# Kernel optimization log

Measured on AMD Instinct MI355X. Metric: run time of the kernel, lower is better.

Reference implementation:

```python
import jax, jax.numpy as jnp
import numpy as np

NUM_NODES = 100000
NUM_EDGES = 1600000
NUM_GRAPHS = 64
IN_CH, HID, NCLS = 15, 128, 11


def setup_inputs() -> dict:
    key = jax.random.key(0)
    ks = jax.random.split(key, 9)
    x = jax.random.normal(ks[0], (NUM_NODES, IN_CH), dtype=jnp.float32)
    edge_index = jax.random.randint(ks[1], (2, NUM_EDGES), 0, NUM_NODES, dtype=jnp.int64)
    batch = jnp.sort(jax.random.randint(ks[2], (NUM_NODES,), 0, NUM_GRAPHS, dtype=jnp.int64))
    s1 = 1.0 / np.sqrt(IN_CH)
    s2 = 1.0 / np.sqrt(HID)
    W1 = jax.random.normal(ks[3], (IN_CH, HID), dtype=jnp.float32) * s1
    b1 = jax.random.normal(ks[4], (HID,), dtype=jnp.float32) * s1
    W2 = jax.random.normal(ks[5], (HID, HID), dtype=jnp.float32) * s2
    b2 = jax.random.normal(ks[6], (HID,), dtype=jnp.float32) * s2
    Wf = jax.random.normal(ks[7], (HID, NCLS), dtype=jnp.float32) * s2
    bf = jax.random.normal(ks[8], (NCLS,), dtype=jnp.float32) * s2
    return {"x": x, "edge_index": edge_index, "batch": batch,
            "W1": W1, "b1": b1, "W2": W2, "b2": b2, "Wf": Wf, "bf": bf}


def reference(x, edge_index, batch, W1, b1, W2, b2, Wf, bf):
    N = x.shape[0]
    loop = jnp.arange(N, dtype=edge_index.dtype)
    # PyG GCNConv: add self-loops, symmetric D^{-1/2} A D^{-1/2} normalization
    src = jnp.concatenate([edge_index[0], loop])
    dst = jnp.concatenate([edge_index[1], loop])
    deg = jax.ops.segment_sum(jnp.ones(src.shape[0], dtype=x.dtype), dst, num_segments=N)
    dinv = deg ** -0.5  # deg >= 1 due to self-loops
    norm = (dinv[src] * dinv[dst])[:, None]  # [E+N, 1]

    def gcn(h, W, b):
        m = h @ W                                   # transform first (smaller gather)
        agg = jax.ops.segment_sum(m[src] * norm, dst, num_segments=N)
        return agg + b

    h = jax.nn.relu(gcn(x, W1, b1))
    h = jax.nn.relu(gcn(h, W2, b2))

    # global_mean_pool over graph ids
    sums = jax.ops.segment_sum(h, batch, num_segments=NUM_GRAPHS)
    cnts = jax.ops.segment_sum(jnp.ones((N,), dtype=h.dtype), batch, num_segments=NUM_GRAPHS)
    pooled = sums / jnp.maximum(cnts, 1.0)[:, None]  # [G, HID]
    return pooled @ Wf + bf                          # [G, NCLS]
```

## Files before the change

### kernel.cpp

```cpp
#include <hip/hip_runtime.h>

#define N_NODES 100000
#define N_EDGES 1600000
#define N_GRAPHS 64
#define IN_CH 15
#define HID 128
#define NCLS 11

#define NBUCK 196
#define NBF 512
#define EPB (N_EDGES / NBF)

using short8 = __attribute__((ext_vector_type(8))) short;
using f32x4 = __attribute__((ext_vector_type(4))) float;
using f32x2 = __attribute__((ext_vector_type(2))) float;

__device__ __forceinline__ unsigned short f2bf(float f) {
    unsigned u = __builtin_bit_cast(unsigned, f);
    u += 0x7FFF + ((u >> 16) & 1);
    return (unsigned short)(u >> 16);
}
__device__ __forceinline__ unsigned packbf(float a, float b) {
    return (unsigned)f2bf(a) | ((unsigned)f2bf(b) << 16);
}
__device__ __forceinline__ float2 unpackbf(unsigned v) {
    float2 r;
    unsigned lo = v << 16;
    unsigned hi = v & 0xFFFF0000u;
    r.x = __builtin_bit_cast(float, lo);
    r.y = __builtin_bit_cast(float, hi);
    return r;
}

__device__ __forceinline__ unsigned char f2fp8(float f) {
    return (unsigned char)(__builtin_amdgcn_cvt_pk_fp8_f32(f, f, 0, false) & 0xFF);
}

__global__ __launch_bounds__(256) void k_init(float* __restrict__ pooled) {
    int i = blockIdx.x * 256 + threadIdx.x;
    if (i < N_GRAPHS * HID) pooled[i] = 0.f;
}

__global__ __launch_bounds__(256) void k_hist(const int* __restrict__ dst,
                                              int* __restrict__ cntm) {
    __shared__ int hist[NBUCK];
    int t = threadIdx.x;
    for (int i = t; i < NBUCK; i += 256) hist[i] = 0;
    __syncthreads();
    int base = blockIdx.x * EPB;
#pragma unroll
    for (int i = 0; i < (EPB + 255) / 256; ++i) {
        int e = i * 256 + t;
        if (e < EPB) atomicAdd(&hist[dst[base + e] >> 9], 1);
    }
    __syncthreads();
    for (int b = t; b < NBUCK; b += 256)
        cntm[b * NBF + blockIdx.x] = hist[b];
}

__global__ __launch_bounds__(256) void k_btot(const int* __restrict__ cntm,
                                              int* __restrict__ tot) {
    __shared__ int red[256];
    int b = blockIdx.x, t = threadIdx.x;
    red[t] = cntm[b * NBF + t] + cntm[b * NBF + t + 256];
    __syncthreads();
    for (int off = 128; off > 0; off >>= 1) {
        if (t < off) red[t] += red[t + off];
        __syncthreads();
    }
    if (t == 0) tot[b] = red[0];
}

__global__ __launch_bounds__(256) void k_bscan(const int* __restrict__ tot,
                                               int* __restrict__ bbase,
                                               int* __restrict__ rowptr) {
    __shared__ int arr[256];
    int t = threadIdx.x;
    arr[t] = (t < NBUCK) ? tot[t] : 0;
    __syncthreads();
    for (int off = 1; off < 256; off <<= 1) {
        int v = (t >= off) ? arr[t - off] : 0;
        __syncthreads();
        arr[t] += v;
        __syncthreads();
    }
    if (t < NBUCK) bbase[t] = (t == 0) ? 0 : arr[t - 1];
    if (t == 0) rowptr[N_NODES] = N_EDGES;
}

__global__ __launch_bounds__(NBF) void k_offs(const int* __restrict__ cntm,
                                              const int* __restrict__ bbase,
                                              int* __restrict__ offs) {
    __shared__ int arr[NBF];
    int b = blockIdx.x, t = threadIdx.x;
    arr[t] = cntm[b * NBF + t];
    __syncthreads();
    for (int off = 1; off < NBF; off <<= 1) {
        int v = (t >= off) ? arr[t - off] : 0;
        __syncthreads();
        arr[t] += v;
        __syncthreads();
    }
    offs[b * NBF + t] = bbase[b] + ((t == 0) ? 0 : arr[t - 1]);
}

__global__ __launch_bounds__(256) void k_partition(const int* __restrict__ src,
                                                   const int* __restrict__ dst,
                                                   const int* __restrict__ offs,
                                                   unsigned* __restrict__ staging) {
    __shared__ int cur[NBUCK];
    int t = threadIdx.x;
    for (int b = t; b < NBUCK; b += 256) cur[b] = offs[b * NBF + blockIdx.x];
    __syncthreads();
    int base = blockIdx.x * EPB;
#pragma unroll
    for (int i = 0; i < (EPB + 255) / 256; ++i) {
        int e = i * 256 + t;
        if (e < EPB) {
            int d = dst[base + e];
            int s = src[base + e];
            int slot = atomicAdd(&cur[d >> 9], 1);
            staging[slot] = ((unsigned)(d & 511) << 17) | (unsigned)s;
        }
    }
}

__global__ __launch_bounds__(256) void k_fuse(const unsigned* __restrict__ staging,
                                              const int* __restrict__ bbase,
                                              int* __restrict__ rowptr,
                                              float* __restrict__ dinv,
                                              int* __restrict__ csr_src) {
    __shared__ int cnt[512];
    __shared__ int cur[512];
    __shared__ int arr[256];
    int b = blockIdx.x, t = threadIdx.x;
    cnt[t] = 0; cnt[t + 256] = 0;
    __syncthreads();
    int beg = bbase[b];
    int end = (b == NBUCK - 1) ? N_EDGES : bbase[b + 1];
    for (int e = beg + t; e < end; e += 256)
        atomicAdd(&cnt[staging[e] >> 17], 1);
    __syncthreads();
    int c0 = cnt[2 * t], c1 = cnt[2 * t + 1];
    arr[t] = c0 + c1;
    __syncthreads();
    for (int off = 1; off < 256; off <<= 1) {
        int v = (t >= off) ? arr[t - off] : 0;
        __syncthreads();
        arr[t] += v;
        __syncthreads();
    }
    int excl = (t == 0) ? 0 : arr[t - 1];
    int p0 = beg + excl;
    int p1 = p0 + c0;
    cur[2 * t] = p0;
    cur[2 * t + 1] = p1;
    int n0 = b << 9;
    int n = n0 + 2 * t;
    if (n < N_NODES) { rowptr[n] = p0; dinv[n] = rsqrtf((float)(c0 + 1)); }
    n = n0 + 2 * t + 1;
    if (n < N_NODES) { rowptr[n] = p1; dinv[n] = rsqrtf((float)(c1 + 1)); }
    __syncthreads();
    for (int e = beg + t; e < end; e += 256) {
        unsigned v = staging[e];
        int pos = atomicAdd(&cur[v >> 17], 1);
        csr_src[pos] = (int)(v & 0x1FFFFu);
    }
}

__global__ __launch_bounds__(256) void k_w2pack(const float* __restrict__ W2,
                                                uint4* __restrict__ Bp) {
    int i = blockIdx.x * 256 + threadIdx.x;
    if (i >= 2048) return;
    int lane = i & 63;
    int kb = (i >> 6) & 3;
    int ct = i >> 8;
    int col = ct * 16 + (lane & 15);
    int k0 = kb * 32 + ((lane >> 4) & 3) * 8;
    unsigned w[4];
#pragma unroll
    for (int p = 0; p < 4; ++p) {
        int k = k0 + 2 * p;
        w[p] = packbf(W2[k * HID + col], W2[(k + 1) * HID + col]);
    }
    Bp[i] = make_uint4(w[0], w[1], w[2], w[3]);
}

__global__ __launch_bounds__(256) void k_prescale(const float* __restrict__ x,
                                                  const float* __restrict__ dinv,
                                                  unsigned* __restrict__ xs) {
    int i = blockIdx.x * 256 + threadIdx.x;
    if (i >= N_NODES * 8) return;
    int n = i >> 3, p = i & 7;
    float dv = dinv[n];
    int c0 = 2 * p, c1 = c0 + 1;
    float a = x[(size_t)n * IN_CH + c0] * dv;
    float b = (c1 < IN_CH) ? x[(size_t)n * IN_CH + c1] * dv : 0.f;
    xs[i] = packbf(a, b);
}

__global__ __launch_bounds__(256) void k_gather15(const int* __restrict__ rowptr,
                                                  const int* __restrict__ csr_src,
                                                  const unsigned* __restrict__ xs,
                                                  const float* __restrict__ dinv,
                                                  float* __restrict__ agg) {
    int wave = (blockIdx.x * 256 + threadIdx.x) >> 6;
    if (wave >= N_NODES) return;
    int n = wave;
    int l = threadIdx.x & 63;
    unsigned g = (unsigned)(l >> 3), cp = (unsigned)(l & 7);
    int beg = rowptr[n], end = rowptr[n + 1];
    float2 acc = make_float2(0.f, 0.f);
    for (int e = beg + (int)g; e < end; e += 8) {
        unsigned s = (unsigned)csr_src[e];
        float2 v = unpackbf(xs[s * 8u + cp]);
        acc.x += v.x; acc.y += v.y;
    }
#pragma unroll
    for (int off = 8; off < 64; off <<= 1) {
        acc.x += __shfl_xor(acc.x, off, 64);
        acc.y += __shfl_xor(acc.y, off, 64);
    }
    if (l < 8) {
        float2 s = unpackbf(xs[(unsigned)n * 8u + (unsigned)l]);
        float dv = dinv[n];
        float2 r = make_float2((acc.x + s.x) * dv, (acc.y + s.y) * dv);
        *(float2*)&agg[(unsigned)n * 16u + 2u * (unsigned)l] = r;
    }
}

__global__ __launch_bounds__(256) void k_xform1b(const float* __restrict__ agg,
                                                 const float* __restrict__ W1,
                                                 const float* __restrict__ b1,
                                                 unsigned* __restrict__ h1b) {
    __shared__ float w[IN_CH * HID];
    int t = threadIdx.x;
    for (int i = t; i < IN_CH * HID; i += 256) w[i] = W1[i];
    __syncthreads();
    int node = blockIdx.x * 4 + (t >> 6);
    int lane = t & 63;
    int c = lane * 2;
    const float* ar = agg + (size_t)node * 16;
    float a0 = b1[c], a1 = b1[c + 1];
#pragma unroll
    for (int k = 0; k < IN_CH; ++k) {
        float av = ar[k];
        a0 += av * w[k * HID + c];
        a1 += av * w[k * HID + c + 1];
    }
    h1b[(size_t)node * 64 + lane] = packbf(fmaxf(a0, 0.f), fmaxf(a1, 0.f));
}

__global__ __launch_bounds__(256) void k_xform2(const unsigned* __restrict__ h1b,
                                                const uint4* __restrict__ Bp,
                                                const float* __restrict__ dinv,
                                                unsigned char* __restrict__ mout) {
    int lane = threadIdx.x & 63;
    int wid = threadIdx.x >> 6;
    int row0 = blockIdx.x * 64 + wid * 16;
    int arow = row0 + (lane & 15);
    const uint4* hbase = (const uint4*)h1b;
    uint4 a_u[4];
#pragma unroll
    for (int kb = 0; kb < 4; ++kb)
        a_u[kb] = hbase[(size_t)arow * 16 + kb * 4 + (lane >> 4)];
    int rbase = row0 + (lane >> 4) * 4;
    float dv[4];
#pragma unroll
    for (int j = 0; j < 4; ++j) dv[j] = dinv[min(rbase + j, N_NODES - 1)];
#pragma unroll
    for (int ct = 0; ct < 8; ++ct) {
        f32x4 acc = {0.f, 0.f, 0.f, 0.f};
#pragma unroll
        for (int kb = 0; kb < 4; ++kb) {
            uint4 b_u = Bp[(ct * 4 + kb) * 64 + lane];
            acc = __builtin_amdgcn_mfma_f32_16x16x32_bf16(
                __builtin_bit_cast(short8, a_u[kb]),
                __builtin_bit_cast(short8, b_u), acc, 0, 0, 0);
        }
        int col = ct * 16 + (lane & 15);
#pragma unroll
        for (int j = 0; j < 4; ++j) {
            int r = rbase + j;
            if (r < N_NODES) mout[(size_t)r * HID + col] = f2fp8(acc[j] * dv[j]);
        }
    }
}

__global__ __launch_bounds__(256) void k_gather(const int* __restrict__ rowptr,
                                                const int* __restrict__ csr_src,
                                                const unsigned* __restrict__ m,
                                                const float* __restrict__ bias,
                                                const float* __restrict__ dinv,
                                                unsigned* __restrict__ outh) {
    int wave = (blockIdx.x * 256 + threadIdx.x) >> 6;
    if (wave >= N_NODES) return;
    unsigned n = (unsigned)wave;
    int lane = threadIdx.x & 63;
    int half = lane >> 5;
    unsigned li = (unsigned)(lane & 31);
    int beg = rowptr[n], end = rowptr[n + 1];
    f32x4 acc = {0.f, 0.f, 0.f, 0.f};
    if (half == 0) {
        unsigned u = m[n * 32u + li];
        f32x2 lo = __builtin_amdgcn_cvt_pk_f32_fp8((int)u, false);
        f32x2 hi = __builtin_amdgcn_cvt_pk_f32_fp8((int)u, true);
        acc[0] += lo[0]; acc[1] += lo[1]; acc[2] += hi[0]; acc[3] += hi[1];
    }
    int e = beg + half;
    for (; e + 6 < end; e += 8) {
        unsigned o0 = (unsigned)csr_src[e + 0] * 32u + li;
        unsigned o1 = (unsigned)csr_src[e + 2] * 32u + li;
        unsigned o2 = (unsigned)csr_src[e + 4] * 32u + li;
        unsigned o3 = (unsigned)csr_src[e + 6] * 32u + li;
        unsigned u0 = m[o0];
        unsigned u1 = m[o1];
        unsigned u2 = m[o2];
        unsigned u3 = m[o3];
        f32x2 l0 = __builtin_amdgcn_cvt_pk_f32_fp8((int)u0, false);
        f32x2 h0 = __builtin_amdgcn_cvt_pk_f32_fp8((int)u0, true);
        f32x2 l1 = __builtin_amdgcn_cvt_pk_f32_fp8((int)u1, false);
        f32x2 h1 = __builtin_amdgcn_cvt_pk_f32_fp8((int)u1, true);
        f32x2 l2 = __builtin_amdgcn_cvt_pk_f32_fp8((int)u2, false);
        f32x2 h2 = __builtin_amdgcn_cvt_pk_f32_fp8((int)u2, true);
        f32x2 l3 = __builtin_amdgcn_cvt_pk_f32_fp8((int)u3, false);
        f32x2 h3 = __builtin_amdgcn_cvt_pk_f32_fp8((int)u3, true);
        acc[0] += l0[0] + l1[0] + l2[0] + l3[0];
        acc[1] += l0[1] + l1[1] + l2[1] + l3[1];
        acc[2] += h0[0] + h1[0] + h2[0] + h3[0];
        acc[3] += h0[1] + h1[1] + h2[1] + h3[1];
    }
    for (; e < end; e += 2) {
        unsigned u = m[(unsigned)csr_src[e] * 32u + li];
        f32x2 lo = __builtin_amdgcn_cvt_pk_f32_fp8((int)u, false);
        f32x2 hi = __builtin_amdgcn_cvt_pk_f32_fp8((int)u, true);
        acc[0] += lo[0]; acc[1] += lo[1]; acc[2] += hi[0]; acc[3] += hi[1];
    }
#pragma unroll
    for (int j = 0; j < 4; ++j) acc[j] += __shfl_xor(acc[j], 32, 64);
    if (half == 0) {
        float dv = dinv[n];
        float4 b = *(const float4*)&bias[li * 4u];
        float r0 = fmaxf(acc[0] * dv + b.x, 0.f);
        float r1 = fmaxf(acc[1] * dv + b.y, 0.f);
        float r2 = fmaxf(acc[2] * dv + b.z, 0.f);
        float r3 = fmaxf(acc[3] * dv + b.w, 0.f);
        uint2 ov;
        ov.x = packbf(r0, r1);
        ov.y = packbf(r2, r3);
        *(uint2*)&outh[n * 64u + li * 2u] = ov;
    }
}

__global__ __launch_bounds__(64) void k_cnt(const int* __restrict__ batch,
                                            int* __restrict__ cnt) {
    int g = threadIdx.x;
    if (g >= N_GRAPHS) return;
    int lo0 = 0, hi0 = N_NODES;
    while (lo0 < hi0) { int mid = (lo0 + hi0) >> 1; if (batch[mid] < g) lo0 = mid + 1; else hi0 = mid; }
    int lo1 = lo0, hi1 = N_NODES;
    while (lo1 < hi1) { int mid = (lo1 + hi1) >> 1; if (batch[mid] < g + 1) lo1 = mid + 1; else hi1 = mid; }
    cnt[g] = lo1 - lo0;
}

#define POOL_CHUNK 128
__global__ __launch_bounds__(256) void k_pool(const unsigned* __restrict__ h,
                                              const int* __restrict__ batch,
                                              float* __restrict__ pooled) {
    int t = threadIdx.x;
    int lane = t & 63;
    int grp = t >> 6;
    int start = blockIdx.x * POOL_CHUNK;
    int end = min(start + POOL_CHUNK, N_NODES);
    float2 acc = make_float2(0.f, 0.f);
    int cur = -1;
    for (int n = start + grp; n < end; n += 4) {
        int g = batch[n];
        if (g != cur) {
            if (cur >= 0) {
                atomicAdd(&pooled[cur * HID + lane * 2], acc.x);
                atomicAdd(&pooled[cur * HID + lane * 2 + 1], acc.y);
            }
            acc = make_float2(0.f, 0.f);
            cur = g;
        }
        float2 v = unpackbf(h[(unsigned)n * 64u + (unsigned)lane]);
        acc.x += v.x; acc.y += v.y;
    }
    if (cur >= 0) {
        atomicAdd(&pooled[cur * HID + lane * 2], acc.x);
        atomicAdd(&pooled[cur * HID + lane * 2 + 1], acc.y);
    }
}

__global__ __launch_bounds__(128) void k_final(const float* __restrict__ pooled,
                                               const int* __restrict__ cnt,
                                               const float* __restrict__ Wf,
                                               const float* __restrict__ bf,
                                               float* __restrict__ out) {
    __shared__ float p[HID];
    int g = blockIdx.x, t = threadIdx.x;
    float inv = 1.f / fmaxf((float)cnt[g], 1.f);
    p[t] = pooled[g * HID + t] * inv;
    __syncthreads();
    if (t < NCLS) {
        float acc = bf[t];
        for (int k = 0; k < HID; ++k) acc += p[k] * Wf[k * NCLS + t];
        out[g * NCLS + t] = acc;
    }
}

extern "C" void kernel_launch(void* const* d_in, const int* in_sizes, int n_in,
                              void* d_out, int out_size, void* d_ws, size_t ws_size,
                              hipStream_t stream) {
    const float* x   = (const float*)d_in[0];
    const int*   ei  = (const int*)d_in[1];
    const int*   src = ei;
    const int*   dst = ei + N_EDGES;
    const int*   batch = (const int*)d_in[2];
    const float* W1 = (const float*)d_in[3];
    const float* b1 = (const float*)d_in[4];
    const float* W2 = (const float*)d_in[5];
    const float* b2 = (const float*)d_in[6];
    const float* Wf = (const float*)d_in[7];
    const float* bf = (const float*)d_in[8];
    float* out = (float*)d_out;

    char* ws = (char*)d_ws;
    size_t off = 0;
    unsigned* mbuf = (unsigned*)(ws + off);  off += (size_t)N_NODES * 64 * 4;
    unsigned* h1b = (unsigned*)(ws + off);   off += (size_t)N_NODES * 64 * 4;
    unsigned* h2b = (unsigned*)(ws + off);   off += (size_t)N_NODES * 64 * 4;
    int* csr_src = (int*)(ws + off);         off += (size_t)N_EDGES * 4;
    uint4* Bp = (uint4*)(ws + off);          off += (size_t)2048 * 16;
    float* dinv = (float*)(ws + off);        off += (size_t)N_NODES * 4;
    int* rowptr = (int*)(ws + off);          off += (size_t)(N_NODES + 1) * 4;
    int* cntm = (int*)(ws + off);            off += (size_t)NBUCK * NBF * 4;
    int* offs = (int*)(ws + off);            off += (size_t)NBUCK * NBF * 4;
    int* tot = (int*)(ws + off);             off += (size_t)NBUCK * 4;
    int* bbase = (int*)(ws + off);           off += (size_t)NBUCK * 4;
    float* pooled = (float*)(ws + off);      off += (size_t)N_GRAPHS * HID * 4;
    int* cnt = (int*)(ws + off);             off += (size_t)N_GRAPHS * 4;
    unsigned* staging = h2b;
    unsigned* xs = mbuf;
    float* agg = (float*)(mbuf + (size_t)N_NODES * 8);
    unsigned char* mfp8 = (unsigned char*)mbuf;

    k_init<<<(N_GRAPHS * HID + 255) / 256, 256, 0, stream>>>(pooled);
    k_hist<<<NBF, 256, 0, stream>>>(dst, cntm);
    k_btot<<<NBUCK, 256, 0, stream>>>(cntm, tot);
    k_bscan<<<1, 256, 0, stream>>>(tot, bbase, rowptr);
    k_offs<<<NBUCK, NBF, 0, stream>>>(cntm, bbase, offs);
    k_partition<<<NBF, 256, 0, stream>>>(src, dst, offs, staging);
    k_fuse<<<NBUCK, 256, 0, stream>>>(staging, bbase, rowptr, dinv, csr_src);
    k_w2pack<<<8, 256, 0, stream>>>(W2, Bp);

    k_prescale<<<(N_NODES * 8 + 255) / 256, 256, 0, stream>>>(x, dinv, xs);
    k_gather15<<<(N_NODES + 3) / 4, 256, 0, stream>>>(rowptr, csr_src, xs, dinv, agg);
    k_xform1b<<<N_NODES / 4, 256, 0, stream>>>(agg, W1, b1, h1b);

    k_xform2<<<(N_NODES + 63) / 64, 256, 0, stream>>>(h1b, Bp, dinv, mfp8);
    k_gather<<<(N_NODES + 3) / 4, 256, 0, stream>>>(rowptr, csr_src, (const unsigned*)mfp8, b2, dinv, h2b);

    k_cnt<<<1, 64, 0, stream>>>(batch, cnt);
    k_pool<<<(N_NODES + POOL_CHUNK - 1) / POOL_CHUNK, 256, 0, stream>>>(h2b, batch, pooled);
    k_final<<<N_GRAPHS, 128, 0, stream>>>(pooled, cnt, Wf, bf, out);
}
```

Baseline: 235.1 us.

## Fuse layer-1 gather with W1 transform and fold small kernels into neighbors

Merges the 15-channel neighbor gather and the 15x128 W1 transform into one kernel: after the wave reduction, lanes broadcast the aggregated features with shuffles and each lane computes two output channels from W1 held in registers. This drops the intermediate agg buffer round trip and one launch. The pooled zero-init moves into the scan kernel, and the per-graph count binary search moves into the final kernel, removing two more tiny launches. Each wave now loads W1 into registers itself, which raises register use and repeats weight loads per node.

```diff
diff --git a/kernel.cpp b/kernel.cpp
--- a/kernel.cpp
+++ b/kernel.cpp
@@ -36,11 +36,6 @@
     return (unsigned char)(__builtin_amdgcn_cvt_pk_fp8_f32(f, f, 0, false) & 0xFF);
 }
 
-__global__ __launch_bounds__(256) void k_init(float* __restrict__ pooled) {
-    int i = blockIdx.x * 256 + threadIdx.x;
-    if (i < N_GRAPHS * HID) pooled[i] = 0.f;
-}
-
 __global__ __launch_bounds__(256) void k_hist(const int* __restrict__ dst,
                                               int* __restrict__ cntm) {
     __shared__ int hist[NBUCK];
@@ -73,7 +68,8 @@
 
 __global__ __launch_bounds__(256) void k_bscan(const int* __restrict__ tot,
                                                int* __restrict__ bbase,
-                                               int* __restrict__ rowptr) {
+                                               int* __restrict__ rowptr,
+                                               float* __restrict__ pooled) {
     __shared__ int arr[256];
     int t = threadIdx.x;
     arr[t] = (t < NBUCK) ? tot[t] : 0;
@@ -86,6 +82,7 @@
     }
     if (t < NBUCK) bbase[t] = (t == 0) ? 0 : arr[t - 1];
     if (t == 0) rowptr[N_NODES] = N_EDGES;
+    for (int i = t; i < N_GRAPHS * HID; i += 256) pooled[i] = 0.f;
 }
 
 __global__ __launch_bounds__(NBF) void k_offs(const int* __restrict__ cntm,
@@ -199,19 +196,26 @@
     xs[i] = packbf(a, b);
 }
 
-__global__ __launch_bounds__(256) void k_gather15(const int* __restrict__ rowptr,
-                                                  const int* __restrict__ csr_src,
-                                                  const unsigned* __restrict__ xs,
-                                                  const float* __restrict__ dinv,
-                                                  float* __restrict__ agg) {
+__global__ __launch_bounds__(256) void k_l1fused(const int* __restrict__ rowptr,
+                                                 const int* __restrict__ csr_src,
+                                                 const unsigned* __restrict__ xs,
+                                                 const float* __restrict__ dinv,
+                                                 const float* __restrict__ W1,
+                                                 const float* __restrict__ b1,
+                                                 unsigned* __restrict__ h1b) {
     int wave = (blockIdx.x * 256 + threadIdx.x) >> 6;
     if (wave >= N_NODES) return;
-    int n = wave;
+    unsigned n = (unsigned)wave;
     int l = threadIdx.x & 63;
-    unsigned g = (unsigned)(l >> 3), cp = (unsigned)(l & 7);
+    int g = l >> 3;
+    unsigned cp = (unsigned)(l & 7);
+    float2 w[IN_CH];
+#pragma unroll
+    for (int k = 0; k < IN_CH; ++k) w[k] = *(const float2*)&W1[k * HID + l * 2];
+    float2 bb = *(const float2*)&b1[l * 2];
     int beg = rowptr[n], end = rowptr[n + 1];
     float2 acc = make_float2(0.f, 0.f);
-    for (int e = beg + (int)g; e < end; e += 8) {
+    for (int e = beg + g; e < end; e += 8) {
         unsigned s = (unsigned)csr_src[e];
         float2 v = unpackbf(xs[s * 8u + cp]);
         acc.x += v.x; acc.y += v.y;
@@ -221,34 +225,21 @@
         acc.x += __shfl_xor(acc.x, off, 64);
         acc.y += __shfl_xor(acc.y, off, 64);
     }
-    if (l < 8) {
-        float2 s = unpackbf(xs[(unsigned)n * 8u + (unsigned)l]);
-        float dv = dinv[n];
-        float2 r = make_float2((acc.x + s.x) * dv, (acc.y + s.y) * dv);
-        *(float2*)&agg[(unsigned)n * 16u + 2u * (unsigned)l] = r;
-    }
-}
-
-__global__ __launch_bounds__(256) void k_xform1b(const float* __restrict__ agg,
-                                                 const float* __restrict__ W1,
-                                                 const float* __restrict__ b1,
-                                                 unsigned* __restrict__ h1b) {
-    __shared__ float w[IN_CH * HID];
-    int t = threadIdx.x;
-    for (int i = t; i < IN_CH * HID; i += 256) w[i] = W1[i];
-    __syncthreads();
-    int node = blockIdx.x * 4 + (t >> 6);
-    int lane = t & 63;
-    int c = lane * 2;
-    const float* ar = agg + (size_t)node * 16;
-    float a0 = b1[c], a1 = b1[c + 1];
-#pragma unroll
-    for (int k = 0; k < IN_CH; ++k) {
-        float av = ar[k];
-        a0 += av * w[k * HID + c];
-        a1 += av * w[k * HID + c + 1];
-    }
-    h1b[(size_t)node * 64 + lane] = packbf(fmaxf(a0, 0.f), fmaxf(a1, 0.f));
+    float2 s = unpackbf(xs[n * 8u + cp]);
+    float dv = dinv[n];
+    float ax = (acc.x + s.x) * dv;
+    float ay = (acc.y + s.y) * dv;
+    float a0 = bb.x, a1 = bb.y;
+    int gbase = l & 56;
+#pragma unroll
+    for (int p = 0; p < 8; ++p) {
+        float vx = __shfl(ax, gbase | p, 64);
+        float vy = __shfl(ay, gbase | p, 64);
+        int k0 = 2 * p;
+        a0 += vx * w[k0].x; a1 += vx * w[k0].y;
+        if (k0 + 1 < IN_CH) { a0 += vy * w[k0 + 1].x; a1 += vy * w[k0 + 1].y; }
+    }
+    h1b[(size_t)n * 64 + l] = packbf(fmaxf(a0, 0.f), fmaxf(a1, 0.f));
 }
 
 __global__ __launch_bounds__(256) void k_xform2(const unsigned* __restrict__ h1b,
@@ -350,17 +341,6 @@
         ov.y = packbf(r2, r3);
         *(uint2*)&outh[n * 64u + li * 2u] = ov;
     }
-}
-
-__global__ __launch_bounds__(64) void k_cnt(const int* __restrict__ batch,
-                                            int* __restrict__ cnt) {
-    int g = threadIdx.x;
-    if (g >= N_GRAPHS) return;
-    int lo0 = 0, hi0 = N_NODES;
-    while (lo0 < hi0) { int mid = (lo0 + hi0) >> 1; if (batch[mid] < g) lo0 = mid + 1; else hi0 = mid; }
-    int lo1 = lo0, hi1 = N_NODES;
-    while (lo1 < hi1) { int mid = (lo1 + hi1) >> 1; if (batch[mid] < g + 1) lo1 = mid + 1; else hi1 = mid; }
-    cnt[g] = lo1 - lo0;
 }
 
 #define POOL_CHUNK 128
@@ -394,13 +374,21 @@
 }
 
 __global__ __launch_bounds__(128) void k_final(const float* __restrict__ pooled,
-                                               const int* __restrict__ cnt,
+                                               const int* __restrict__ batch,
                                                const float* __restrict__ Wf,
                                                const float* __restrict__ bf,
                                                float* __restrict__ out) {
     __shared__ float p[HID];
+    __shared__ int bnd[2];
     int g = blockIdx.x, t = threadIdx.x;
-    float inv = 1.f / fmaxf((float)cnt[g], 1.f);
+    if (t < 2) {
+        int key = g + t;
+        int lo = 0, hi = N_NODES;
+        while (lo < hi) { int mid = (lo + hi) >> 1; if (batch[mid] < key) lo = mid + 1; else hi = mid; }
+        bnd[t] = lo;
+    }
+    __syncthreads();
+    float inv = 1.f / fmaxf((float)(bnd[1] - bnd[0]), 1.f);
     p[t] = pooled[g * HID + t] * inv;
     __syncthreads();
     if (t < NCLS) {
@@ -440,29 +428,25 @@
     int* tot = (int*)(ws + off);             off += (size_t)NBUCK * 4;
     int* bbase = (int*)(ws + off);           off += (size_t)NBUCK * 4;
     float* pooled = (float*)(ws + off);      off += (size_t)N_GRAPHS * HID * 4;
-    int* cnt = (int*)(ws + off);             off += (size_t)N_GRAPHS * 4;
     unsigned* staging = h2b;
-    unsigned* xs = mbuf;
-    float* agg = (float*)(mbuf + (size_t)N_NODES * 8);
+    unsigned* xs = mbuf + (size_t)N_NODES * 16;
+    xs = mbuf + ((size_t)N_NODES * 64 - (size_t)N_NODES * 8);
     unsigned char* mfp8 = (unsigned char*)mbuf;
 
-    k_init<<<(N_GRAPHS * HID + 255) / 256, 256, 0, stream>>>(pooled);
     k_hist<<<NBF, 256, 0, stream>>>(dst, cntm);
     k_btot<<<NBUCK, 256, 0, stream>>>(cntm, tot);
-    k_bscan<<<1, 256, 0, stream>>>(tot, bbase, rowptr);
+    k_bscan<<<1, 256, 0, stream>>>(tot, bbase, rowptr, pooled);
     k_offs<<<NBUCK, NBF, 0, stream>>>(cntm, bbase, offs);
     k_partition<<<NBF, 256, 0, stream>>>(src, dst, offs, staging);
     k_fuse<<<NBUCK, 256, 0, stream>>>(staging, bbase, rowptr, dinv, csr_src);
     k_w2pack<<<8, 256, 0, stream>>>(W2, Bp);
 
     k_prescale<<<(N_NODES * 8 + 255) / 256, 256, 0, stream>>>(x, dinv, xs);
-    k_gather15<<<(N_NODES + 3) / 4, 256, 0, stream>>>(rowptr, csr_src, xs, dinv, agg);
-    k_xform1b<<<N_NODES / 4, 256, 0, stream>>>(agg, W1, b1, h1b);
+    k_l1fused<<<(N_NODES + 3) / 4, 256, 0, stream>>>(rowptr, csr_src, xs, dinv, W1, b1, h1b);
 
     k_xform2<<<(N_NODES + 63) / 64, 256, 0, stream>>>(h1b, Bp, dinv, mfp8);
     k_gather<<<(N_NODES + 3) / 4, 256, 0, stream>>>(rowptr, csr_src, (const unsigned*)mfp8, b2, dinv, h2b);
 
-    k_cnt<<<1, 64, 0, stream>>>(batch, cnt);
     k_pool<<<(N_NODES + POOL_CHUNK - 1) / POOL_CHUNK, 256, 0, stream>>>(h2b, batch, pooled);
-    k_final<<<N_GRAPHS, 128, 0, stream>>>(pooled, cnt, Wf, bf, out);
-}
+    k_final<<<N_GRAPHS, 128, 0, stream>>>(pooled, batch, Wf, bf, out);
+}
```

Result: faster. 215.5 us (-8.3%).
